# Performance work log

Hardware: AMD Instinct MI355X
Metric: run time of the kernel (lower is better)

## Reference

```python
import jax, jax.numpy as jnp
import numpy as np

HIDDEN = 2048
GAMMA = 0.96875
SCALE_BASE = 512  # XPOS default from torchscale / Jamie-Stirling/RetNet


def _xpos(x, downscale=False):
    # x: [B, L, d]. Faithful port of XPOS with offset=0.
    B, L, d = x.shape
    half = d // 2
    # per-dim scale vector: (arange(0,d,2) + 0.4d) / (1.4d)
    scale_vec = (jnp.arange(0, d, 2, dtype=jnp.float32) + 0.4 * d) / (1.4 * d)  # [half]
    power = jnp.arange(L, dtype=jnp.float32) / SCALE_BASE                        # [L]
    scale = scale_vec[None, :] ** power[:, None]                                 # [L, half]
    # fixed_pos_embedding over `half` frequency dims
    inv_freq = 1.0 / (10000.0 ** (jnp.arange(half, dtype=jnp.float32) / half))   # [half]
    sinusoid = jnp.arange(L, dtype=jnp.float32)[:, None] * inv_freq[None, :]     # [L, half]
    sin, cos = jnp.sin(sinusoid), jnp.cos(sinusoid)
    if downscale:
        scale = 1.0 / scale
    # duplicate_interleave: [L, half] -> [L, d] with each column repeated twice
    sin_s = jnp.repeat(sin * scale, 2, axis=-1)  # [L, d]
    cos_s = jnp.repeat(cos * scale, 2, axis=-1)  # [L, d]
    # rotate_every_two
    x1 = x[..., 0::2]
    x2 = x[..., 1::2]
    rot = jnp.stack((-x2, x1), axis=-1).reshape(x.shape)
    return x * cos_s[None] + rot * sin_s[None]


def _decay_matrix(L):
    n = jnp.arange(L)[:, None]
    m = jnp.arange(L)[None, :]
    mask = n >= m
    # clamp exponent to avoid overflow where masked (torch sets NaN->0)
    D = jnp.where(mask, GAMMA ** jnp.maximum(n - m, 0).astype(jnp.float32), 0.0)
    return D  # [L, L]


def setup_inputs() -> dict:
    key = jax.random.key(0)
    kx, kq, kk, kv = jax.random.split(key, 4)
    B, S, H = 4, 2048, HIDDEN
    X = jax.random.normal(kx, (B, S, H), dtype=jnp.float32)
    W_Q = jax.random.normal(kq, (H, H), dtype=jnp.float32) / H
    W_K = jax.random.normal(kk, (H, H), dtype=jnp.float32) / H
    W_V = jax.random.normal(kv, (H, H), dtype=jnp.float32) / H
    return {"X": X, "W_Q": W_Q, "W_K": W_K, "W_V": W_V}


def reference(X, W_Q, W_K, W_V):
    B, S, H = X.shape
    Q = _xpos(X @ W_Q)                   # [B, S, H]
    K = _xpos(X @ W_K, downscale=True)   # [B, S, H]
    V = X @ W_V                          # [B, S, H]
    D = _decay_matrix(S)                 # [S, S]
    att = jnp.einsum("bnh,bmh->bnm", Q, K) * D[None]  # [B, S, S]
    return att @ V                       # [B, S, H]
```

## Files before the change

kernel.cpp:

```cpp
#include <hip/hip_runtime.h>
#include <math.h>


typedef __attribute__((ext_vector_type(8))) short short8;
typedef __attribute__((ext_vector_type(4))) float f32x4;
typedef __attribute__((ext_vector_type(4))) unsigned short us4;

#define BM 128
#define BK 64

static __device__ __forceinline__ unsigned short f2bf(float f) {
    unsigned int u = __float_as_uint(f);
    u += 0x7FFFu + ((u >> 16) & 1u);
    return (unsigned short)(u >> 16);
}

static __device__ __forceinline__ void gload16(const unsigned short* g, unsigned short* l) {
    __builtin_amdgcn_global_load_lds(
        (const __attribute__((address_space(1))) unsigned int*)g,
        (__attribute__((address_space(3))) unsigned int*)l, 16, 0, 0);
}

template <int STAGE, int BNt>
__global__ __launch_bounds__(256)
void gemm_bt(const unsigned short* __restrict__ A,
             const unsigned short* __restrict__ Bt,
             void* __restrict__ Cv,
             unsigned short* __restrict__ Cq,
             unsigned short* __restrict__ Ck,
             unsigned short* __restrict__ Cvt,
             int lda, int ldb, int Kd,
             long long sA, long long sB, long long sC)
{
    constexpr int S = 2048, H = 2048;
    constexpr int NJ = BNt / 32;
    constexpr int QB = BNt / 32;

    int bx, by, zb;
    if (STAGE == 3) {
        int t = blockIdx.x;
        if (t < 12) {
            by = (t < 2) ? 0 : (t < 6) ? 1 : 2;
            bx = t - ((by == 0) ? 0 : (by == 1) ? 2 : 6);
        } else {
            by = 3 + (t - 12) / 8;
            bx = (2 * by - 6) + ((t - 12) & 7);
        }
        zb = blockIdx.z;
    } else if (STAGE == 4) {
        bx = blockIdx.x;
        by = (int)gridDim.z - 1 - (int)blockIdx.z;
        zb = blockIdx.y;
    } else {
        bx = blockIdx.x; by = blockIdx.y; zb = 0;
    }
    const int rowBase = by * BM;
    const int colBase = bx * BNt;

    A  += (long long)zb * sA;
    Bt += (long long)zb * sB;

    __shared__ unsigned short As[BM * BK];
    __shared__ unsigned short Bs[BNt * BK];

    const int tid  = threadIdx.x;
    const int wave = tid >> 6;
    const int lane = tid & 63;
    const int wm = (wave & 1) * 64;
    const int wn = (wave >> 1) * (BNt / 2);

    f32x4 acc[4][NJ];
#pragma unroll
    for (int i = 0; i < 4; ++i)
#pragma unroll
        for (int j = 0; j < NJ; ++j) acc[i][j] = (f32x4){0.f, 0.f, 0.f, 0.f};

    int kmax = Kd;
    if (STAGE == 4) { int km = rowBase + BM; kmax = km < Kd ? km : Kd; }
    int k0s = 0;
    if (STAGE == 4) { int kb0 = 2 * by - 6; k0s = (kb0 > 0 ? kb0 : 0) * 64; }

    const int lr8 = lane >> 3;
    const int schunk = ((lane & 7) ^ (lr8 & 7)) * 8;
    const unsigned short* ga = A  + (size_t)(rowBase + wave * 32 + lr8) * lda + schunk;
    const unsigned short* gb = Bt + (size_t)(colBase + wave * (BNt / 4) + lr8) * ldb + schunk;
    unsigned short* lA = As + wave * 2048;
    unsigned short* lB = Bs + wave * (BNt * 16);

#pragma unroll
    for (int q = 0; q < 4; ++q) gload16(ga + k0s + (size_t)q * 8 * lda, lA + q * 512);
#pragma unroll
    for (int q = 0; q < QB; ++q) gload16(gb + k0s + (size_t)q * 8 * ldb, lB + q * 512);

    const int fr = lane & 15;
    const int qd = lane >> 4;
    const int fsw = fr & 7;

    for (int k0 = k0s; k0 < kmax; k0 += BK) {
        __syncthreads();
        short8 af0[4], af1[4], bf0[NJ], bf1[NJ];
#pragma unroll
        for (int i = 0; i < 4; ++i) {
            int row = wm + i * 16 + fr;
            af0[i] = *(const short8*)&As[row * 64 + ((qd ^ fsw) * 8)];
            af1[i] = *(const short8*)&As[row * 64 + (((4 + qd) ^ fsw) * 8)];
        }
#pragma unroll
        for (int j = 0; j < NJ; ++j) {
            int row = wn + j * 16 + fr;
            bf0[j] = *(const short8*)&Bs[row * 64 + ((qd ^ fsw) * 8)];
            bf1[j] = *(const short8*)&Bs[row * 64 + (((4 + qd) ^ fsw) * 8)];
        }
        __syncthreads();
        if (k0 + BK < kmax) {
            const unsigned short* ga2 = ga + k0 + BK;
            const unsigned short* gb2 = gb + k0 + BK;
#pragma unroll
            for (int q = 0; q < 4; ++q) gload16(ga2 + (size_t)q * 8 * lda, lA + q * 512);
#pragma unroll
            for (int q = 0; q < QB; ++q) gload16(gb2 + (size_t)q * 8 * ldb, lB + q * 512);
        }
#pragma unroll
        for (int i = 0; i < 4; ++i)
#pragma unroll
            for (int j = 0; j < NJ; ++j)
                acc[i][j] = __builtin_amdgcn_mfma_f32_16x16x32_bf16(af0[i], bf0[j], acc[i][j], 0, 0, 0);
#pragma unroll
        for (int i = 0; i < 4; ++i)
#pragma unroll
            for (int j = 0; j < NJ; ++j)
                acc[i][j] = __builtin_amdgcn_mfma_f32_16x16x32_bf16(af1[i], bf1[j], acc[i][j], 0, 0, 0);
    }

    if (STAGE == 1) {
        const int mode = colBase >> 11;
        if (mode < 2) {
            unsigned short* Co = (mode == 0) ? Cq : Ck;
            const float psgn = (mode == 1) ? -1.953125e-3f : 1.953125e-3f;
#pragma unroll
            for (int j = 0; j < NJ; ++j) {
                int gc = (colBase & 2047) + wn + j * 16 + fr;
                float c0 = (float)(gc & ~1);
                float l2sv = log2f((c0 + 819.2f) * (1.0f / 2867.2f)) * psgn;
                float invf = exp2f(c0 * -0.0064881407f);
                float s1, c1;
                sincosf(invf, &s1, &c1);
#pragma unroll
                for (int i = 0; i < 4; ++i) {
                    int gr0 = rowBase + wm + i * 16 + qd * 4;
                    float fn = (float)(gr0 & (S - 1));
                    float sN, cN;
                    sincosf(fn * invf, &sN, &cN);
#pragma unroll
                    for (int r = 0; r < 4; ++r) {
                        float scale = exp2f(fn * l2sv);
                        float cs = cN * scale, ss = sN * scale;
                        float v = acc[i][j][r];
                        float o = __shfl_xor(v, 1);
                        float res = (gc & 1) ? fmaf(v, cs, o * ss) : fmaf(v, cs, -o * ss);
                        Co[(size_t)(gr0 + r) * H + gc] = f2bf(res);
                        float sn2 = sN * c1 + cN * s1;
                        cN = cN * c1 - sN * s1;
                        sN = sn2;
                        fn += 1.0f;
                    }
                }
            }
        } else {
#pragma unroll
            for (int j = 0; j < NJ; ++j) {
                int gh = (colBase & 2047) + wn + j * 16 + fr;
#pragma unroll
                for (int i = 0; i < 4; ++i) {
                    int gm0 = rowBase + wm + i * 16 + qd * 4;
                    us4 p;
#pragma unroll
                    for (int r = 0; r < 4; ++r) p[r] = f2bf(acc[i][j][r]);
                    *(us4*)&Cvt[(size_t)gh * 8192 + gm0] = p;
                }
            }
        }
    } else if (STAGE == 3) {
        unsigned short* att = (unsigned short*)Cv + (long long)zb * sC;
#pragma unroll
        for (int j = 0; j < NJ; ++j) {
            int m = colBase + wn + j * 16 + fr;
#pragma unroll
            for (int i = 0; i < 4; ++i) {
                int n0 = rowBase + wm + i * 16 + qd * 4;
#pragma unroll
                for (int r = 0; r < 4; ++r) {
                    int d = n0 + r - m;
                    float v = (d >= 0) ? acc[i][j][r] * exp2f((float)d * -0.045803598f) : 0.0f;
                    att[(size_t)(n0 + r) * S + m] = f2bf(v);
                }
            }
        }
    } else {
        float* Co = (float*)Cv + (long long)zb * sC;
#pragma unroll
        for (int j = 0; j < NJ; ++j) {
            int gh = colBase + wn + j * 16 + fr;
#pragma unroll
            for (int i = 0; i < 4; ++i) {
                int gn0 = rowBase + wm + i * 16 + qd * 4;
#pragma unroll
                for (int r = 0; r < 4; ++r)
                    Co[(size_t)(gn0 + r) * H + gh] = acc[i][j][r];
            }
        }
    }
}

__global__ __launch_bounds__(256)
void cvt_f32_bf16(const float* __restrict__ x, unsigned short* __restrict__ y) {
    int i = blockIdx.x * 256 + threadIdx.x;
    float4 v = ((const float4*)x)[i];
    us4 o = {f2bf(v.x), f2bf(v.y), f2bf(v.z), f2bf(v.w)};
    ((us4*)y)[i] = o;
}

__global__ __launch_bounds__(256)
void cvt_transpose3(const float* __restrict__ W0, const float* __restrict__ W1,
                    const float* __restrict__ W2, unsigned short* __restrict__ Wt) {
    __shared__ float t[64][65];
    const float* W = (blockIdx.z == 0) ? W0 : (blockIdx.z == 1) ? W1 : W2;
    unsigned short* Wo = Wt + (size_t)blockIdx.z * 4194304;
    int bx = blockIdx.x * 64, by = blockIdx.y * 64;
    int tx = threadIdx.x & 63, ty = threadIdx.x >> 6;
#pragma unroll
    for (int r = 0; r < 64; r += 4)
        t[ty + r][tx] = W[(size_t)(by + ty + r) * 2048 + bx + tx];
    __syncthreads();
#pragma unroll
    for (int r = 0; r < 64; r += 4)
        Wo[(size_t)(bx + ty + r) * 2048 + by + tx] = f2bf(t[tx][ty + r]);
}

extern "C" void kernel_launch(void* const* d_in, const int* in_sizes, int n_in,
                              void* d_out, int out_size, void* d_ws, size_t ws_size,
                              hipStream_t stream) {
    const int S = 2048, H = 2048;
    const long long MH = 16777216;
    const long long HH = 4194304;
    const long long SH = (long long)S * H;
    const long long SS = (long long)S * S;

    const float* X  = (const float*)d_in[0];
    const float* WQ = (const float*)d_in[1];
    const float* WK = (const float*)d_in[2];
    const float* WV = (const float*)d_in[3];
    float* out = (float*)d_out;

    unsigned short* Xb    = (unsigned short*)d_ws;
    unsigned short* WtAll = Xb + MH;
    unsigned short* Qb    = WtAll + 3 * HH;
    unsigned short* Kb    = Qb + MH;
    unsigned short* Vt    = Kb + MH;
    unsigned short* att   = Vt + MH;

    cvt_f32_bf16<<<16384, 256, 0, stream>>>(X, Xb);
    cvt_transpose3<<<dim3(32, 32, 3), 256, 0, stream>>>(WQ, WK, WV, WtAll);

    gemm_bt<1, 128><<<dim3(48, 64), 256, 0, stream>>>(Xb, WtAll, nullptr, Qb, Kb, Vt,
                                                      H, H, H, 0, 0, 0);
    gemm_bt<3, 64><<<dim3(116, 1, 4), 256, 0, stream>>>(Qb, Kb, att, nullptr, nullptr, nullptr,
                                                        H, H, H, SH, SH, SS);
    gemm_bt<4, 128><<<dim3(16, 4, 16), 256, 0, stream>>>(att, Vt, out, nullptr, nullptr, nullptr,
                                                         S, 8192, S, SS, 2048, SH);
}
```

Before: 449.7 us.

## Swizzle block order for XCD locality and fuse conversion kernels

The stage-3 and stage-4 GEMMs move to flat 1D grids. Block IDs are remapped so that consecutive IDs, which are dealt round-robin across the 8 XCDs, fall into contiguous tile ranges on each XCD. This is meant to improve L2 reuse of shared A/B tiles. The X conversion and the weight transpose-conversion are also merged into one launch, with X handled as 8 elements per thread, to save a kernel launch and widen stores. The swizzle depends on the hardware dispatch order, and the mapping must still cover every tile exactly once.

```diff
diff --git a/kernel.cpp b/kernel.cpp
--- a/kernel.cpp
+++ b/kernel.cpp
@@ -38,7 +38,10 @@
 
     int bx, by, zb;
     if (STAGE == 3) {
-        int t = blockIdx.x;
+        int id = blockIdx.x;
+        int swz = (id & 7) * 58 + (id >> 3);
+        zb = swz / 116;
+        int t = swz - zb * 116;
         if (t < 12) {
             by = (t < 2) ? 0 : (t < 6) ? 1 : 2;
             bx = t - ((by == 0) ? 0 : (by == 1) ? 2 : 6);
@@ -46,11 +49,13 @@
             by = 3 + (t - 12) / 8;
             bx = (2 * by - 6) + ((t - 12) & 7);
         }
-        zb = blockIdx.z;
     } else if (STAGE == 4) {
-        bx = blockIdx.x;
-        by = (int)gridDim.z - 1 - (int)blockIdx.z;
-        zb = blockIdx.y;
+        int id = blockIdx.x;
+        int swz = (id & 7) * 128 + (id >> 3);
+        bx = swz >> 6;
+        int r = swz & 63;
+        zb = r >> 4;
+        by = 15 - (r & 15);
     } else {
         bx = blockIdx.x; by = blockIdx.y; zb = 0;
     }
@@ -213,28 +218,39 @@
 }
 
 __global__ __launch_bounds__(256)
-void cvt_f32_bf16(const float* __restrict__ x, unsigned short* __restrict__ y) {
-    int i = blockIdx.x * 256 + threadIdx.x;
-    float4 v = ((const float4*)x)[i];
-    us4 o = {f2bf(v.x), f2bf(v.y), f2bf(v.z), f2bf(v.w)};
-    ((us4*)y)[i] = o;
-}
-
-__global__ __launch_bounds__(256)
-void cvt_transpose3(const float* __restrict__ W0, const float* __restrict__ W1,
-                    const float* __restrict__ W2, unsigned short* __restrict__ Wt) {
+void cvt_fused(const float* __restrict__ X, unsigned short* __restrict__ Xb,
+               const float* __restrict__ W0, const float* __restrict__ W1,
+               const float* __restrict__ W2, unsigned short* __restrict__ Wt) {
     __shared__ float t[64][65];
-    const float* W = (blockIdx.z == 0) ? W0 : (blockIdx.z == 1) ? W1 : W2;
-    unsigned short* Wo = Wt + (size_t)blockIdx.z * 4194304;
-    int bx = blockIdx.x * 64, by = blockIdx.y * 64;
-    int tx = threadIdx.x & 63, ty = threadIdx.x >> 6;
-#pragma unroll
-    for (int r = 0; r < 64; r += 4)
-        t[ty + r][tx] = W[(size_t)(by + ty + r) * 2048 + bx + tx];
-    __syncthreads();
-#pragma unroll
-    for (int r = 0; r < 64; r += 4)
-        Wo[(size_t)(bx + ty + r) * 2048 + by + tx] = f2bf(t[tx][ty + r]);
+    if (blockIdx.x < 3072) {
+        int id = blockIdx.x;
+        int z = id >> 10, rem = id & 1023;
+        const float* W = (z == 0) ? W0 : (z == 1) ? W1 : W2;
+        unsigned short* Wo = Wt + (size_t)z * 4194304;
+        int bx = (rem & 31) * 64, by = (rem >> 5) * 64;
+        int tx = threadIdx.x & 63, ty = threadIdx.x >> 6;
+#pragma unroll
+        for (int r = 0; r < 64; r += 4)
+            t[ty + r][tx] = W[(size_t)(by + ty + r) * 2048 + bx + tx];
+        __syncthreads();
+#pragma unroll
+        for (int r = 0; r < 64; r += 4)
+            Wo[(size_t)(bx + ty + r) * 2048 + by + tx] = f2bf(t[tx][ty + r]);
+    } else {
+        int id = blockIdx.x - 3072;
+        const float4* X4 = (const float4*)X;
+        short8* O8 = (short8*)Xb;
+#pragma unroll
+        for (int c = 0; c < 4; ++c) {
+            size_t u = (size_t)c * (2048 * 256) + (size_t)id * 256 + threadIdx.x;
+            float4 a = X4[u * 2];
+            float4 b = X4[u * 2 + 1];
+            short8 o;
+            o[0] = f2bf(a.x); o[1] = f2bf(a.y); o[2] = f2bf(a.z); o[3] = f2bf(a.w);
+            o[4] = f2bf(b.x); o[5] = f2bf(b.y); o[6] = f2bf(b.z); o[7] = f2bf(b.w);
+            O8[u] = o;
+        }
+    }
 }
 
 extern "C" void kernel_launch(void* const* d_in, const int* in_sizes, int n_in,
@@ -259,13 +275,12 @@
     unsigned short* Vt    = Kb + MH;
     unsigned short* att   = Vt + MH;
 
-    cvt_f32_bf16<<<16384, 256, 0, stream>>>(X, Xb);
-    cvt_transpose3<<<dim3(32, 32, 3), 256, 0, stream>>>(WQ, WK, WV, WtAll);
+    cvt_fused<<<5120, 256, 0, stream>>>(X, Xb, WQ, WK, WV, WtAll);
 
     gemm_bt<1, 128><<<dim3(48, 64), 256, 0, stream>>>(Xb, WtAll, nullptr, Qb, Kb, Vt,
                                                       H, H, H, 0, 0, 0);
-    gemm_bt<3, 64><<<dim3(116, 1, 4), 256, 0, stream>>>(Qb, Kb, att, nullptr, nullptr, nullptr,
+    gemm_bt<3, 64><<<dim3(464, 1, 1), 256, 0, stream>>>(Qb, Kb, att, nullptr, nullptr, nullptr,
                                                         H, H, H, SH, SH, SS);
-    gemm_bt<4, 128><<<dim3(16, 4, 16), 256, 0, stream>>>(att, Vt, out, nullptr, nullptr, nullptr,
-                                                         S, 8192, S, SS, 2048, SH);
-}
+    gemm_bt<4, 128><<<dim3(1024, 1, 1), 256, 0, stream>>>(att, Vt, out, nullptr, nullptr, nullptr,
+                                                          S, 8192, S, SS, 2048, SH);
+}
```

Result: faster. 422.6 us (-6.0%).
